# Optimization experiments

Hardware: AMD Instinct MI355X
Metric: run time of the kernel (lower is better)

Reference implementation:

```python
import jax, jax.numpy as jnp
import numpy as np

N = 120000   # hits
K = 512      # non-noise objects (ids 1..K; id 0 = noise)
D = 8        # cluster-space dim
C = 6        # pid classes
Q_MIN = 1.0
NOISE_THR = 0
PAYLOAD_W = 1.0
EPS = 1e-9


def setup_inputs() -> dict:
    key = jax.random.key(0)
    ks = jax.random.split(key, 9)
    beta = jax.random.uniform(ks[0], (N,), dtype=jnp.float32) * 0.95 + 0.01  # keep arctanh finite
    x = jax.random.normal(ks[1], (N, D), dtype=jnp.float32)
    object_id = jax.random.randint(ks[2], (N,), 0, K + 1).astype(jnp.int32)
    # guarantee every object id (and noise id 0) appears at least once
    object_id = object_id.at[: K + 1].set(jnp.arange(K + 1, dtype=jnp.int32))
    energy = jax.random.normal(ks[3], (N,), dtype=jnp.float32)
    energy_per_hit = jax.random.normal(ks[4], (N,), dtype=jnp.float32)
    momentum = jax.random.normal(ks[5], (N, 3), dtype=jnp.float32)
    momentum_per_hit = jax.random.normal(ks[6], (N, 3), dtype=jnp.float32)
    pid_logits = jax.random.normal(ks[7], (N, C), dtype=jnp.float32)
    pid_per_hit = jax.random.randint(ks[8], (N,), 0, C).astype(jnp.int32)
    return dict(beta=beta, x=x, object_id=object_id, energy=energy,
                energy_per_hit=energy_per_hit, momentum=momentum,
                momentum_per_hit=momentum_per_hit, pid_logits=pid_logits,
                pid_per_hit=pid_per_hit)


def _oc_core(beta, x, object_id):
    """condensation_loss_tiger with weights=1, max_n_rep=0 (no repulsive sampling)."""
    oids = jnp.arange(1, K + 1, dtype=object_id.dtype)
    att_mask = object_id[:, None] == oids[None, :]              # [N, K]
    q = jnp.arctanh(beta) ** 2 + Q_MIN                          # [N]
    alphas = jnp.argmax(q[:, None] * att_mask, axis=0)          # [K] condensation points
    x_k = x[alphas]                                             # [K, D]
    q_k = q[alphas]                                             # [K]
    # squared euclidean distance via gemm (avoids [N,K,D] intermediate)
    d2 = (jnp.sum(x * x, axis=1)[:, None] + jnp.sum(x_k * x_k, axis=1)[None, :]
          - 2.0 * (x @ x_k.T))
    d2 = jnp.maximum(d2, 0.0)                                   # [N, K]
    dist = jnp.sqrt(jnp.maximum(d2, 1e-12))
    qw = q[:, None] * q_k[None, :]                              # [N, K]
    # attractive: per-object normalized by hits in object, then mean over objects
    att_norm = jnp.sum(att_mask, axis=0).astype(x.dtype)        # [K]
    v_att = jnp.sum(jnp.where(att_mask, qw * d2, 0.0) / (att_norm + EPS)[None, :]) / K
    # repulsive: hinge (1 - dist), normalized by n_hits not in object
    rep_mask = (~att_mask) & (dist < 1.0)
    n_rep_k = jnp.sum(~att_mask, axis=0).astype(x.dtype)        # [K]
    n_rep = jnp.sum(rep_mask)
    v_rep = jnp.sum(jnp.where(rep_mask, qw * (1.0 - dist), 0.0) / (n_rep_k + EPS)[None, :]) / K
    l_coward = jnp.mean(1.0 - beta[alphas])
    noise_m = (object_id <= NOISE_THR).astype(beta.dtype)
    l_noise = jnp.sum(beta * noise_m) / jnp.sum(noise_m)
    return v_att, v_rep, l_coward, l_noise, n_rep


def reference(beta, x, object_id, energy, energy_per_hit, momentum,
              momentum_per_hit, pid_logits, pid_per_hit):
    v_att, v_rep, l_coward, l_noise, n_rep = _oc_core(beta, x, object_id)
    oc_total = v_att + v_rep + l_coward + l_noise
    # payload losses on non-noise hits (masked means == F.*_loss on gathered rows)
    m = (object_id > NOISE_THR).astype(beta.dtype)              # [N]
    nm = jnp.sum(m)
    e_loss = jnp.sum((energy - energy_per_hit) ** 2 * m) / nm
    p_loss = jnp.sum((momentum - momentum_per_hit) ** 2 * m[:, None]) / (nm * momentum.shape[1])
    logp = jax.nn.log_softmax(pid_logits, axis=-1)              # [N, C]
    nll = -jnp.take_along_axis(logp, pid_per_hit[:, None], axis=1)[:, 0]
    pid_loss = jnp.sum(nll * m) / nm
    total = oc_total + PAYLOAD_W * (e_loss + p_loss + pid_loss)
    return (v_att, v_rep, l_coward, l_noise, n_rep.astype(jnp.float32),
            oc_total, e_loss, p_loss, pid_loss, total)
```

## Files before the change

### kernel.cpp

```cpp
#include <hip/hip_runtime.h>
#include <math.h>

#define KOBJ 512
#define KTW 8
#define TK 32
#define NTILE (KOBJ / TK)
#define HB 8
#define HCH (256 * HB)
#define MPREP 256
#define GB 64

typedef _Float16 half2_t __attribute__((ext_vector_type(2)));

#define AGS(p, v) __hip_atomic_store((p), (v), __ATOMIC_RELAXED, __HIP_MEMORY_SCOPE_AGENT)
#define AGL(p)    __hip_atomic_load((p), __ATOMIC_RELAXED, __HIP_MEMORY_SCOPE_AGENT)

__device__ __forceinline__ float wave_red_f(float v) {
  #pragma unroll
  for (int off = 32; off > 0; off >>= 1) v += __shfl_down(v, off, 64);
  return v;
}

__device__ __forceinline__ float q_of_beta(float b) {
  float a = 0.5f * __logf((1.f + b) / (1.f - b));
  return fmaf(a, a, 1.f);
}

__device__ __forceinline__ float dot8h(uint4 kx, const uint* y, float acc) {
#if __has_builtin(__builtin_amdgcn_fdot2)
  acc = __builtin_amdgcn_fdot2(__builtin_bit_cast(half2_t, y[0]),
                               __builtin_bit_cast(half2_t, kx.x), acc, false);
  acc = __builtin_amdgcn_fdot2(__builtin_bit_cast(half2_t, y[1]),
                               __builtin_bit_cast(half2_t, kx.y), acc, false);
  acc = __builtin_amdgcn_fdot2(__builtin_bit_cast(half2_t, y[2]),
                               __builtin_bit_cast(half2_t, kx.z), acc, false);
  acc = __builtin_amdgcn_fdot2(__builtin_bit_cast(half2_t, y[3]),
                               __builtin_bit_cast(half2_t, kx.w), acc, false);
#else
  const uint kk[4] = {kx.x, kx.y, kx.z, kx.w};
  #pragma unroll
  for (int c = 0; c < 4; c++) {
    half2_t a = __builtin_bit_cast(half2_t, y[c]);
    half2_t b = __builtin_bit_cast(half2_t, kk[c]);
    acc = fmaf((float)a.x, (float)b.x, acc);
    acc = fmaf((float)a.y, (float)b.y, acc);
  }
#endif
  return acc;
}

__global__ __launch_bounds__(256) void
k_prep(const float* __restrict__ beta, const float* __restrict__ x,
       const int* __restrict__ oid,
       const float* __restrict__ energy, const float* __restrict__ eph,
       const float* __restrict__ mom, const float* __restrict__ mph,
       const float* __restrict__ logits, const int* __restrict__ pid,
       unsigned long long* __restrict__ amax_part,
       unsigned* __restrict__ cnt_part,
       float* __restrict__ scal_part,
       uint4* __restrict__ hry, uint4* __restrict__ hrm,
       unsigned* __restrict__ done_cnt, int n) {
  __shared__ unsigned long long lmax[KOBJ];
  __shared__ unsigned lcnt[KOBJ];
  if (blockIdx.x == 0 && threadIdx.x == 0) *done_cnt = 0u;
  for (int t = threadIdx.x; t < KOBJ; t += 256) { lmax[t] = 0ull; lcnt[t] = 0u; }
  __syncthreads();

  const float4* xp = (const float4*)x;
  float e_t = 0.f, p_t = 0.f, pid_t = 0.f, noise_t = 0.f, ncnt = 0.f, mcnt = 0.f;
  for (int i = blockIdx.x * 256 + threadIdx.x; i < n; i += MPREP * 256) {
    float b = beta[i];
    int o = oid[i];
    float q = q_of_beta(b);
    float4 xa = xp[2 * (size_t)i];
    float4 xb = xp[2 * (size_t)i + 1];
    float xi[8] = {xa.x, xa.y, xa.z, xa.w, xb.x, xb.y, xb.z, xb.w};
    float s = 0.f;
    #pragma unroll
    for (int c = 0; c < 8; c++) s = fmaf(xi[c], xi[c], s);
    uint4 r0;
    {
      half2_t h0 = { (_Float16)(-2.f * xi[0]), (_Float16)(-2.f * xi[1]) };
      half2_t h1 = { (_Float16)(-2.f * xi[2]), (_Float16)(-2.f * xi[3]) };
      half2_t h2 = { (_Float16)(-2.f * xi[4]), (_Float16)(-2.f * xi[5]) };
      half2_t h3 = { (_Float16)(-2.f * xi[6]), (_Float16)(-2.f * xi[7]) };
      r0.x = __builtin_bit_cast(uint, h0);
      r0.y = __builtin_bit_cast(uint, h1);
      r0.z = __builtin_bit_cast(uint, h2);
      r0.w = __builtin_bit_cast(uint, h3);
    }
    uint4 r1 = { __float_as_uint(s), __float_as_uint(q), (uint)o, 0u };
    hry[i] = r0;
    hrm[i] = r1;

    if (o > 0) {
      unsigned long long key = ((unsigned long long)__float_as_uint(q) << 32)
                             | (unsigned long long)(unsigned)(~(unsigned)i);
      atomicMax(&lmax[o - 1], key);
      atomicAdd(&lcnt[o - 1], 1u);
      mcnt += 1.f;
      float de = energy[i] - eph[i];
      e_t = fmaf(de, de, e_t);
      float p0 = mom[3*i+0] - mph[3*i+0];
      float p1 = mom[3*i+1] - mph[3*i+1];
      float p2 = mom[3*i+2] - mph[3*i+2];
      p_t = fmaf(p0, p0, p_t); p_t = fmaf(p1, p1, p_t); p_t = fmaf(p2, p2, p_t);
      const float* lg = logits + 6*i;
      float l0=lg[0], l1=lg[1], l2=lg[2], l3=lg[3], l4=lg[4], l5=lg[5];
      float mx = fmaxf(fmaxf(fmaxf(l0,l1),fmaxf(l2,l3)), fmaxf(l4,l5));
      float sm = __expf(l0-mx)+__expf(l1-mx)+__expf(l2-mx)
               + __expf(l3-mx)+__expf(l4-mx)+__expf(l5-mx);
      int pc = pid[i];
      float lp = (pc==0)?l0:(pc==1)?l1:(pc==2)?l2:(pc==3)?l3:(pc==4)?l4:l5;
      pid_t += mx + __logf(sm) - lp;
    } else {
      noise_t += b;
      ncnt += 1.f;
    }
  }
  __syncthreads();

  for (int t = threadIdx.x; t < KOBJ; t += 256) {
    amax_part[(size_t)blockIdx.x * KOBJ + t] = lmax[t];
    cnt_part[(size_t)blockIdx.x * KOBJ + t]  = lcnt[t];
  }

  float vals[6] = {e_t, p_t, pid_t, noise_t, ncnt, mcnt};
  #pragma unroll
  for (int j = 0; j < 6; j++) vals[j] = wave_red_f(vals[j]);
  __shared__ float sred[4][6];
  int w = threadIdx.x >> 6, l = threadIdx.x & 63;
  if (l == 0) {
    #pragma unroll
    for (int j = 0; j < 6; j++) sred[w][j] = vals[j];
  }
  __syncthreads();
  if (threadIdx.x == 0) {
    #pragma unroll
    for (int j = 0; j < 6; j++)
      scal_part[blockIdx.x * 8 + j] = sred[0][j]+sred[1][j]+sred[2][j]+sred[3][j];
  }
}

__global__ __launch_bounds__(256) void
k_gather(const float* __restrict__ x, const float* __restrict__ beta,
         const unsigned long long* __restrict__ amax_part,
         const unsigned* __restrict__ cnt_part,
         uint* __restrict__ ktab, float* __restrict__ cow_part, int n) {
  __shared__ unsigned long long skey[32][8];
  __shared__ unsigned scnt[32][8];
  const int o = threadIdx.x & 7, seg = threadIdx.x >> 3;
  const int k = blockIdx.x * 8 + o;

  unsigned long long key = 0ull;
  unsigned cnt = 0u;
  for (int m = seg; m < MPREP; m += 32) {
    unsigned long long km = amax_part[(size_t)m * KOBJ + k];
    key = (km > key) ? km : key;
    cnt += cnt_part[(size_t)m * KOBJ + k];
  }
  skey[seg][o] = key;
  scnt[seg][o] = cnt;
  __syncthreads();
  for (int s = 16; s > 0; s >>= 1) {
    if (seg < s) {
      unsigned long long k2 = skey[seg + s][o];
      if (k2 > skey[seg][o]) skey[seg][o] = k2;
      scnt[seg][o] += scnt[seg + s][o];
    }
    __syncthreads();
  }

  float cowv = 0.f;
  if (threadIdx.x < 8) {
    key = skey[0][o];
    cnt = scnt[0][o];
    unsigned idx = ~(unsigned)(key & 0xffffffffull);
    float q_k = __uint_as_float((unsigned)(key >> 32));
    const float4* xp = (const float4*)x;
    float4 xa = xp[2 * (size_t)idx];
    float4 xb = xp[2 * (size_t)idx + 1];
    float xv[8] = {xa.x, xa.y, xa.z, xa.w, xb.x, xb.y, xb.z, xb.w};
    float s2 = 0.f;
    #pragma unroll
    for (int c = 0; c < 8; c++) s2 = fmaf(xv[c], xv[c], s2);
    uint* kt = ktab + (size_t)k * KTW;
    #pragma unroll
    for (int c = 0; c < 4; c++) {
      half2_t hp = { (_Float16)xv[2*c], (_Float16)xv[2*c+1] };
      kt[c] = __builtin_bit_cast(uint, hp);
    }
    kt[4] = __float_as_uint(s2);
    kt[5] = __float_as_uint(q_k / ((float)(n - (int)cnt) + 1e-9f));
    kt[6] = __float_as_uint(q_k / ((float)cnt + 1e-9f));
    kt[7] = 0u;
    cowv = 1.f - beta[idx];
  }
  if (threadIdx.x < 64) {
    cowv = wave_red_f(cowv);
    if (threadIdx.x == 0) cow_part[blockIdx.x] = cowv;
  }
}

__global__ __launch_bounds__(256, 4) void
k_pairs(const uint4* __restrict__ hry, const uint4* __restrict__ hrm,
        const uint* __restrict__ ktab,
        const float* __restrict__ scal_part, const float* __restrict__ cow_part,
        float* __restrict__ pairs_part, unsigned* __restrict__ done_cnt,
        float* __restrict__ out, int n) {
  __shared__ __align__(16) uint skt[(TK + 1) * KTW];
  __shared__ float sredu[4][10];
  __shared__ unsigned slast;
  const int tid = threadIdx.x;
  const int w = tid >> 6, l = tid & 63;
  const int tile0 = blockIdx.y * TK;
  const int hbase = blockIdx.x * HCH;
  const int nblk = gridDim.x * gridDim.y;
  const int bid = blockIdx.y * gridDim.x + blockIdx.x;

  skt[tid] = ktab[(size_t)tile0 * KTW + tid];
  if (tid < KTW) skt[TK * KTW + tid] = 0u;
  __syncthreads();

  uint yh[HB][4];
  float thr[HB], bh[HB], qi[HB];
  int own[HB];
  #pragma unroll
  for (int h = 0; h < HB; h++) {
    int i = hbase + h * 256 + tid;
    if (i < n) {
      uint4 ra = hry[i];
      uint4 rb = hrm[i];
      yh[h][0] = ra.x; yh[h][1] = ra.y; yh[h][2] = ra.z; yh[h][3] = ra.w;
      float s = __uint_as_float(rb.x);
      bh[h] = s;
      thr[h] = 1.f - s;
      qi[h] = __uint_as_float(rb.y);
      own[h] = (int)rb.z - 1 - tile0;
    } else {
      #pragma unroll
      for (int c = 0; c < 4; c++) yh[h][c] = 0u;
      bh[h] = 0.f;
      thr[h] = -1e30f;
      qi[h] = 0.f;
      own[h] = -1;
    }
  }

  float att = 0.f, rep = 0.f, nrep = 0.f;
  const uint4* skt4 = (const uint4*)skt;
  uint4 ka = skt4[0], kb = skt4[1];
  #pragma unroll 2
  for (int r = 0; r < TK; r++) {
    uint4 na = skt4[2*r + 2];
    uint4 nb = skt4[2*r + 3];
    float s2 = __uint_as_float(kb.x);
    float wr = __uint_as_float(kb.y);
    float dp[HB];
    #pragma unroll
    for (int h = 0; h < HB; h++) dp[h] = dot8h(ka, yh[h], s2);
    bool any = false;
    #pragma unroll
    for (int h = 0; h < HB; h++) any = any | (dp[h] < thr[h]);
    if (any) {
      #pragma unroll
      for (int h = 0; h < HB; h++) {
        if (dp[h] < thr[h]) {
          float d2 = dp[h] + bh[h];
          float dist = sqrtf(fmaxf(d2, 1e-12f));
          rep = fmaf(qi[h] * (1.f - dist), wr, rep);
          nrep += 1.f;
        }
      }
    }
    ka = na; kb = nb;
  }

  #pragma unroll
  for (int h = 0; h < HB; h++) {
    int ko = own[h];
    if (ko >= 0 && ko < TK) {
      uint4 oa = skt4[2*ko];
      uint4 ob = skt4[2*ko + 1];
      float s2 = __uint_as_float(ob.x);
      float wr = __uint_as_float(ob.y);
      float wa = __uint_as_float(ob.z);
      float dp = dot8h(oa, yh[h], s2);
      float d2 = dp + bh[h];
      att = fmaf(qi[h] * fmaxf(d2, 0.f), wa, att);
      if (dp < thr[h]) {
        float dist = sqrtf(fmaxf(d2, 1e-12f));
        rep = fmaf(-qi[h] * (1.f - dist), wr, rep);
        nrep -= 1.f;
      }
    }
  }

  att = wave_red_f(att);
  rep = wave_red_f(rep);
  nrep = wave_red_f(nrep);
  if (l == 0) { sredu[w][0] = att; sredu[w][1] = rep; sredu[w][2] = nrep; }
  __syncthreads();
  if (tid == 0) {
    AGS(&pairs_part[bid * 4 + 0], sredu[0][0]+sredu[1][0]+sredu[2][0]+sredu[3][0]);
    AGS(&pairs_part[bid * 4 + 1], sredu[0][1]+sredu[1][1]+sredu[2][1]+sredu[3][1]);
    AGS(&pairs_part[bid * 4 + 2], sredu[0][2]+sredu[1][2]+sredu[2][2]+sredu[3][2]);
    slast = __hip_atomic_fetch_add(done_cnt, 1u, __ATOMIC_ACQ_REL,
                                   __HIP_MEMORY_SCOPE_AGENT);
  }
  __syncthreads();

  if (slast == (unsigned)(nblk - 1)) {
    float v[10] = {0,0,0,0,0,0,0,0,0,0};
    for (int b2 = tid; b2 < nblk; b2 += 256) {
      v[0] += AGL(&pairs_part[b2 * 4 + 0]);
      v[1] += AGL(&pairs_part[b2 * 4 + 1]);
      v[2] += AGL(&pairs_part[b2 * 4 + 2]);
    }
    for (int m = tid; m < MPREP; m += 256) {
      #pragma unroll
      for (int j = 0; j < 6; j++) v[3 + j] += scal_part[m * 8 + j];
    }
    for (int g = tid; g < GB; g += 256) v[9] += cow_part[g];
    #pragma unroll
    for (int j = 0; j < 10; j++) v[j] = wave_red_f(v[j]);
    __syncthreads();
    if (l == 0) {
      #pragma unroll
      for (int j = 0; j < 10; j++) sredu[w][j] = v[j];
    }
    __syncthreads();
    if (tid == 0) {
      float t10[10];
      #pragma unroll
      for (int j = 0; j < 10; j++)
        t10[j] = sredu[0][j]+sredu[1][j]+sredu[2][j]+sredu[3][j];
      float v_att  = t10[0] / (float)KOBJ;
      float v_rep  = t10[1] / (float)KOBJ;
      float n_rep  = t10[2];
      float l_cow  = t10[9] / (float)KOBJ;
      float l_noise = t10[6] / t10[7];
      float oc = v_att + v_rep + l_cow + l_noise;
      float nm = t10[8];
      float e_loss  = t10[3] / nm;
      float p_loss  = t10[4] / (nm * 3.f);
      float pid_loss = t10[5] / nm;
      out[0] = v_att;
      out[1] = v_rep;
      out[2] = l_cow;
      out[3] = l_noise;
      out[4] = n_rep;
      out[5] = oc;
      out[6] = e_loss;
      out[7] = p_loss;
      out[8] = pid_loss;
      out[9] = oc + e_loss + p_loss + pid_loss;
    }
  }
}

extern "C" void kernel_launch(void* const* d_in, const int* in_sizes, int n_in,
                              void* d_out, int out_size, void* d_ws, size_t ws_size,
                              hipStream_t stream) {
  const float* beta   = (const float*)d_in[0];
  const float* x      = (const float*)d_in[1];
  const int*   oid    = (const int*)d_in[2];
  const float* energy = (const float*)d_in[3];
  const float* eph    = (const float*)d_in[4];
  const float* mom    = (const float*)d_in[5];
  const float* mph    = (const float*)d_in[6];
  const float* logits = (const float*)d_in[7];
  const int*   pid    = (const int*)d_in[8];
  float* outp = (float*)d_out;
  const int n = in_sizes[0];
  const int nhb = (n + HCH - 1) / HCH;
  const int nblk_tot = nhb * NTILE;

  char* base = (char*)d_ws;
  size_t off = 0;
  uint*  ktab       = (uint*)(base + off);  off += (size_t)KOBJ * KTW * 4;
  float* cow_part   = (float*)(base + off); off += (size_t)GB * 4;
  float* pairs_part = (float*)(base + off); off += (size_t)nblk_tot * 4 * 4;
  float* scal_part  = (float*)(base + off); off += (size_t)MPREP * 8 * 4;
  unsigned* done_cnt = (unsigned*)(base + off); off += 256;
  off = (off + 255) & ~(size_t)255;
  unsigned long long* amax_part = (unsigned long long*)(base + off); off += (size_t)MPREP * KOBJ * 8;
  unsigned* cnt_part = (unsigned*)(base + off);                      off += (size_t)MPREP * KOBJ * 4;
  off = (off + 255) & ~(size_t)255;
  uint4* hry = (uint4*)(base + off); off += (size_t)nhb * HCH * 16;
  uint4* hrm = (uint4*)(base + off); off += (size_t)nhb * HCH * 16;

  k_prep<<<MPREP, 256, 0, stream>>>(beta, x, oid, energy, eph, mom, mph, logits, pid,
                                    amax_part, cnt_part, scal_part, hry, hrm,
                                    done_cnt, n);
  k_gather<<<GB, 256, 0, stream>>>(x, beta, amax_part, cnt_part, ktab, cow_part, n);
  k_pairs<<<dim3(nhb, NTILE), 256, 0, stream>>>(hry, hrm, ktab, scal_part, cow_part,
                                                pairs_part, done_cnt, outp, n);
}
```

Measured before the change: 112.8 us.

## Drop gather kernel; use replicated global atomic tables and rebuild object table per block

The prep kernel now handles one hit per thread and updates condensation-point argmax keys and per-object counts with global atomics into 8 replicated tables, chosen by block index. This replaces the 256 per-block partial tables that k_gather then reduced. k_gather is removed: each k_pairs block merges the 8 tables for its 32-object tile, gathers the condensation points and builds its shared object table itself, and the coward term is reduced per tile. A memset zeroes the tables and the done counter, which saves one kernel launch and the large partial-table traffic. In exchange it adds global atomic contention and redundant per-block gather work.

Measured after the change: 119.7 us. +6.1%, slower.

```diff
diff --git a/kernel.cpp b/kernel.cpp
--- a/kernel.cpp
+++ b/kernel.cpp
@@ -7,8 +7,7 @@
 #define NTILE (KOBJ / TK)
 #define HB 8
 #define HCH (256 * HB)
-#define MPREP 256
-#define GB 64
+#define NTAB 8
 
 typedef _Float16 half2_t __attribute__((ext_vector_type(2)));
 
@@ -55,23 +54,20 @@
        const float* __restrict__ energy, const float* __restrict__ eph,
        const float* __restrict__ mom, const float* __restrict__ mph,
        const float* __restrict__ logits, const int* __restrict__ pid,
-       unsigned long long* __restrict__ amax_part,
-       unsigned* __restrict__ cnt_part,
+       unsigned long long* __restrict__ amax8,
+       unsigned* __restrict__ cnt8,
        float* __restrict__ scal_part,
-       uint4* __restrict__ hry, uint4* __restrict__ hrm,
-       unsigned* __restrict__ done_cnt, int n) {
-  __shared__ unsigned long long lmax[KOBJ];
-  __shared__ unsigned lcnt[KOBJ];
-  if (blockIdx.x == 0 && threadIdx.x == 0) *done_cnt = 0u;
-  for (int t = threadIdx.x; t < KOBJ; t += 256) { lmax[t] = 0ull; lcnt[t] = 0u; }
-  __syncthreads();
-
-  const float4* xp = (const float4*)x;
+       uint4* __restrict__ hry, uint4* __restrict__ hrm, int n) {
+  const int tid = threadIdx.x;
+  const int i = blockIdx.x * 256 + tid;
+  const int tb = blockIdx.x & (NTAB - 1);
+
   float e_t = 0.f, p_t = 0.f, pid_t = 0.f, noise_t = 0.f, ncnt = 0.f, mcnt = 0.f;
-  for (int i = blockIdx.x * 256 + threadIdx.x; i < n; i += MPREP * 256) {
+  if (i < n) {
     float b = beta[i];
     int o = oid[i];
     float q = q_of_beta(b);
+    const float4* xp = (const float4*)x;
     float4 xa = xp[2 * (size_t)i];
     float4 xb = xp[2 * (size_t)i + 1];
     float xi[8] = {xa.x, xa.y, xa.z, xa.w, xb.x, xb.y, xb.z, xb.w};
@@ -96,119 +92,58 @@
     if (o > 0) {
       unsigned long long key = ((unsigned long long)__float_as_uint(q) << 32)
                              | (unsigned long long)(unsigned)(~(unsigned)i);
-      atomicMax(&lmax[o - 1], key);
-      atomicAdd(&lcnt[o - 1], 1u);
-      mcnt += 1.f;
+      atomicMax(&amax8[(size_t)tb * KOBJ + (o - 1)], key);
+      atomicAdd(&cnt8[(size_t)tb * KOBJ + (o - 1)], 1u);
+      mcnt = 1.f;
       float de = energy[i] - eph[i];
-      e_t = fmaf(de, de, e_t);
+      e_t = de * de;
       float p0 = mom[3*i+0] - mph[3*i+0];
       float p1 = mom[3*i+1] - mph[3*i+1];
       float p2 = mom[3*i+2] - mph[3*i+2];
-      p_t = fmaf(p0, p0, p_t); p_t = fmaf(p1, p1, p_t); p_t = fmaf(p2, p2, p_t);
-      const float* lg = logits + 6*i;
-      float l0=lg[0], l1=lg[1], l2=lg[2], l3=lg[3], l4=lg[4], l5=lg[5];
+      p_t = fmaf(p0, p0, 0.f); p_t = fmaf(p1, p1, p_t); p_t = fmaf(p2, p2, p_t);
+      const float2* lg2 = (const float2*)(logits + 6*i);
+      float2 la = lg2[0], lb = lg2[1], lc = lg2[2];
+      float l0=la.x, l1=la.y, l2=lb.x, l3=lb.y, l4=lc.x, l5=lc.y;
       float mx = fmaxf(fmaxf(fmaxf(l0,l1),fmaxf(l2,l3)), fmaxf(l4,l5));
       float sm = __expf(l0-mx)+__expf(l1-mx)+__expf(l2-mx)
                + __expf(l3-mx)+__expf(l4-mx)+__expf(l5-mx);
       int pc = pid[i];
       float lp = (pc==0)?l0:(pc==1)?l1:(pc==2)?l2:(pc==3)?l3:(pc==4)?l4:l5;
-      pid_t += mx + __logf(sm) - lp;
+      pid_t = mx + __logf(sm) - lp;
     } else {
-      noise_t += b;
-      ncnt += 1.f;
-    }
-  }
-  __syncthreads();
-
-  for (int t = threadIdx.x; t < KOBJ; t += 256) {
-    amax_part[(size_t)blockIdx.x * KOBJ + t] = lmax[t];
-    cnt_part[(size_t)blockIdx.x * KOBJ + t]  = lcnt[t];
+      noise_t = b;
+      ncnt = 1.f;
+    }
   }
 
   float vals[6] = {e_t, p_t, pid_t, noise_t, ncnt, mcnt};
   #pragma unroll
   for (int j = 0; j < 6; j++) vals[j] = wave_red_f(vals[j]);
   __shared__ float sred[4][6];
-  int w = threadIdx.x >> 6, l = threadIdx.x & 63;
+  int w = tid >> 6, l = tid & 63;
   if (l == 0) {
     #pragma unroll
     for (int j = 0; j < 6; j++) sred[w][j] = vals[j];
   }
   __syncthreads();
-  if (threadIdx.x == 0) {
+  if (tid == 0) {
     #pragma unroll
     for (int j = 0; j < 6; j++)
       scal_part[blockIdx.x * 8 + j] = sred[0][j]+sred[1][j]+sred[2][j]+sred[3][j];
   }
 }
 
-__global__ __launch_bounds__(256) void
-k_gather(const float* __restrict__ x, const float* __restrict__ beta,
-         const unsigned long long* __restrict__ amax_part,
-         const unsigned* __restrict__ cnt_part,
-         uint* __restrict__ ktab, float* __restrict__ cow_part, int n) {
-  __shared__ unsigned long long skey[32][8];
-  __shared__ unsigned scnt[32][8];
-  const int o = threadIdx.x & 7, seg = threadIdx.x >> 3;
-  const int k = blockIdx.x * 8 + o;
-
-  unsigned long long key = 0ull;
-  unsigned cnt = 0u;
-  for (int m = seg; m < MPREP; m += 32) {
-    unsigned long long km = amax_part[(size_t)m * KOBJ + k];
-    key = (km > key) ? km : key;
-    cnt += cnt_part[(size_t)m * KOBJ + k];
-  }
-  skey[seg][o] = key;
-  scnt[seg][o] = cnt;
-  __syncthreads();
-  for (int s = 16; s > 0; s >>= 1) {
-    if (seg < s) {
-      unsigned long long k2 = skey[seg + s][o];
-      if (k2 > skey[seg][o]) skey[seg][o] = k2;
-      scnt[seg][o] += scnt[seg + s][o];
-    }
-    __syncthreads();
-  }
-
-  float cowv = 0.f;
-  if (threadIdx.x < 8) {
-    key = skey[0][o];
-    cnt = scnt[0][o];
-    unsigned idx = ~(unsigned)(key & 0xffffffffull);
-    float q_k = __uint_as_float((unsigned)(key >> 32));
-    const float4* xp = (const float4*)x;
-    float4 xa = xp[2 * (size_t)idx];
-    float4 xb = xp[2 * (size_t)idx + 1];
-    float xv[8] = {xa.x, xa.y, xa.z, xa.w, xb.x, xb.y, xb.z, xb.w};
-    float s2 = 0.f;
-    #pragma unroll
-    for (int c = 0; c < 8; c++) s2 = fmaf(xv[c], xv[c], s2);
-    uint* kt = ktab + (size_t)k * KTW;
-    #pragma unroll
-    for (int c = 0; c < 4; c++) {
-      half2_t hp = { (_Float16)xv[2*c], (_Float16)xv[2*c+1] };
-      kt[c] = __builtin_bit_cast(uint, hp);
-    }
-    kt[4] = __float_as_uint(s2);
-    kt[5] = __float_as_uint(q_k / ((float)(n - (int)cnt) + 1e-9f));
-    kt[6] = __float_as_uint(q_k / ((float)cnt + 1e-9f));
-    kt[7] = 0u;
-    cowv = 1.f - beta[idx];
-  }
-  if (threadIdx.x < 64) {
-    cowv = wave_red_f(cowv);
-    if (threadIdx.x == 0) cow_part[blockIdx.x] = cowv;
-  }
-}
-
 __global__ __launch_bounds__(256, 4) void
 k_pairs(const uint4* __restrict__ hry, const uint4* __restrict__ hrm,
-        const uint* __restrict__ ktab,
-        const float* __restrict__ scal_part, const float* __restrict__ cow_part,
+        const unsigned long long* __restrict__ amax8,
+        const unsigned* __restrict__ cnt8,
+        const float* __restrict__ x, const float* __restrict__ beta,
+        const float* __restrict__ scal_part, float* __restrict__ cow_part,
         float* __restrict__ pairs_part, unsigned* __restrict__ done_cnt,
-        float* __restrict__ out, int n) {
+        float* __restrict__ out, int n, int nprep) {
   __shared__ __align__(16) uint skt[(TK + 1) * KTW];
+  __shared__ unsigned long long skey[NTAB][TK];
+  __shared__ unsigned scnt[NTAB][TK];
   __shared__ float sredu[4][10];
   __shared__ unsigned slast;
   const int tid = threadIdx.x;
@@ -218,9 +153,49 @@
   const int nblk = gridDim.x * gridDim.y;
   const int bid = blockIdx.y * gridDim.x + blockIdx.x;
 
-  skt[tid] = ktab[(size_t)tile0 * KTW + tid];
-  if (tid < KTW) skt[TK * KTW + tid] = 0u;
-  __syncthreads();
+  {
+    const int tb = tid >> 5, ko = tid & 31;
+    skey[tb][ko] = amax8[(size_t)tb * KOBJ + tile0 + ko];
+    scnt[tb][ko] = cnt8[(size_t)tb * KOBJ + tile0 + ko];
+    __syncthreads();
+    float cowv = 0.f;
+    if (tid < TK) {
+      unsigned long long key = skey[0][tid];
+      unsigned cnt = scnt[0][tid];
+      #pragma unroll
+      for (int c = 1; c < NTAB; c++) {
+        unsigned long long kc = skey[c][tid];
+        key = (kc > key) ? kc : key;
+        cnt += scnt[c][tid];
+      }
+      unsigned idx = ~(unsigned)(key & 0xffffffffull);
+      float q_k = __uint_as_float((unsigned)(key >> 32));
+      const float4* xp4 = (const float4*)x;
+      float4 xa = xp4[2 * (size_t)idx];
+      float4 xb = xp4[2 * (size_t)idx + 1];
+      float xv[8] = {xa.x, xa.y, xa.z, xa.w, xb.x, xb.y, xb.z, xb.w};
+      float s2 = 0.f;
+      #pragma unroll
+      for (int c = 0; c < 8; c++) s2 = fmaf(xv[c], xv[c], s2);
+      uint* kt = &skt[tid * KTW];
+      #pragma unroll
+      for (int c = 0; c < 4; c++) {
+        half2_t hp = { (_Float16)xv[2*c], (_Float16)xv[2*c+1] };
+        kt[c] = __builtin_bit_cast(uint, hp);
+      }
+      kt[4] = __float_as_uint(s2);
+      kt[5] = __float_as_uint(q_k / ((float)(n - (int)cnt) + 1e-9f));
+      kt[6] = __float_as_uint(q_k / ((float)cnt + 1e-9f));
+      kt[7] = 0u;
+      if (blockIdx.x == 0) cowv = 1.f - beta[idx];
+    }
+    if (tid >= TK && tid < TK + KTW) skt[TK * KTW + (tid - TK)] = 0u;
+    if (tid < 64) {
+      cowv = wave_red_f(cowv);
+      if (tid == 0 && blockIdx.x == 0) AGS(&cow_part[blockIdx.y], cowv);
+    }
+    __syncthreads();
+  }
 
   uint yh[HB][4];
   float thr[HB], bh[HB], qi[HB];
@@ -317,11 +292,11 @@
       v[1] += AGL(&pairs_part[b2 * 4 + 1]);
       v[2] += AGL(&pairs_part[b2 * 4 + 2]);
     }
-    for (int m = tid; m < MPREP; m += 256) {
+    for (int m = tid; m < nprep; m += 256) {
       #pragma unroll
       for (int j = 0; j < 6; j++) v[3 + j] += scal_part[m * 8 + j];
     }
-    for (int g = tid; g < GB; g += 256) v[9] += cow_part[g];
+    for (int g = tid; g < NTILE; g += 256) v[9] += AGL(&cow_part[g]);
     #pragma unroll
     for (int j = 0; j < 10; j++) v[j] = wave_red_f(v[j]);
     __syncthreads();
@@ -373,27 +348,28 @@
   const int*   pid    = (const int*)d_in[8];
   float* outp = (float*)d_out;
   const int n = in_sizes[0];
+  const int nprep = (n + 255) / 256;
   const int nhb = (n + HCH - 1) / HCH;
   const int nblk_tot = nhb * NTILE;
 
   char* base = (char*)d_ws;
   size_t off = 0;
-  uint*  ktab       = (uint*)(base + off);  off += (size_t)KOBJ * KTW * 4;
-  float* cow_part   = (float*)(base + off); off += (size_t)GB * 4;
+  unsigned long long* amax8 = (unsigned long long*)(base + off); off += (size_t)NTAB * KOBJ * 8;
+  unsigned* cnt8     = (unsigned*)(base + off);                  off += (size_t)NTAB * KOBJ * 4;
+  unsigned* done_cnt = (unsigned*)(base + off);                  off += 4;
+  const size_t zero_bytes = off;
+  off = (off + 255) & ~(size_t)255;
+  float* cow_part   = (float*)(base + off); off += (size_t)NTILE * 4;
   float* pairs_part = (float*)(base + off); off += (size_t)nblk_tot * 4 * 4;
-  float* scal_part  = (float*)(base + off); off += (size_t)MPREP * 8 * 4;
-  unsigned* done_cnt = (unsigned*)(base + off); off += 256;
+  float* scal_part  = (float*)(base + off); off += (size_t)nprep * 8 * 4;
   off = (off + 255) & ~(size_t)255;
-  unsigned long long* amax_part = (unsigned long long*)(base + off); off += (size_t)MPREP * KOBJ * 8;
-  unsigned* cnt_part = (unsigned*)(base + off);                      off += (size_t)MPREP * KOBJ * 4;
-  off = (off + 255) & ~(size_t)255;
-  uint4* hry = (uint4*)(base + off); off += (size_t)nhb * HCH * 16;
-  uint4* hrm = (uint4*)(base + off); off += (size_t)nhb * HCH * 16;
-
-  k_prep<<<MPREP, 256, 0, stream>>>(beta, x, oid, energy, eph, mom, mph, logits, pid,
-                                    amax_part, cnt_part, scal_part, hry, hrm,
-                                    done_cnt, n);
-  k_gather<<<GB, 256, 0, stream>>>(x, beta, amax_part, cnt_part, ktab, cow_part, n);
-  k_pairs<<<dim3(nhb, NTILE), 256, 0, stream>>>(hry, hrm, ktab, scal_part, cow_part,
-                                                pairs_part, done_cnt, outp, n);
-}
+  uint4* hry = (uint4*)(base + off); off += (size_t)nprep * 256 * 16;
+  uint4* hrm = (uint4*)(base + off); off += (size_t)nprep * 256 * 16;
+
+  hipMemsetAsync(base, 0, zero_bytes, stream);
+  k_prep<<<nprep, 256, 0, stream>>>(beta, x, oid, energy, eph, mom, mph, logits, pid,
+                                    amax8, cnt8, scal_part, hry, hrm, n);
+  k_pairs<<<dim3(nhb, NTILE), 256, 0, stream>>>(hry, hrm, amax8, cnt8, x, beta,
+                                                scal_part, cow_part, pairs_part,
+                                                done_cnt, outp, n, nprep);
+}
```

## Compute pairwise distance margins with MFMA 32x32x16 f16 instead of fdot2 loops

Applied to the files above, without the earlier changes.

Replaces the per-thread packed-half dot-product loop over the 32 objects in a tile with an MFMA 32x32x16 f16 instruction. Each hit row and object column is augmented so that the matrix product directly yields d2-1, which serves as the repulsion test. Hit data is staged in LDS so lanes can build MFMA fragments, the same-object exclusion moves into the hinge path via a reload of hrm, and launch bounds drop to 3 blocks per SU. The aim is to cut VALU dot-product work, at the cost of more LDS, lower occupancy, f16 rounding of s-1 and s2 in the threshold test, and scattered global reloads when pairs pass the threshold.

Measured after the change: 119.5 us. +5.9%, slower.

```diff
diff --git a/kernel.cpp b/kernel.cpp
--- a/kernel.cpp
+++ b/kernel.cpp
@@ -5,12 +5,13 @@
 #define KTW 8
 #define TK 32
 #define NTILE (KOBJ / TK)
-#define HB 8
-#define HCH (256 * HB)
+#define HCH 2048
 #define MPREP 256
 #define GB 64
 
 typedef _Float16 half2_t __attribute__((ext_vector_type(2)));
+typedef _Float16 f16x8   __attribute__((ext_vector_type(8)));
+typedef float    f32x16  __attribute__((ext_vector_type(16)));
 
 #define AGS(p, v) __hip_atomic_store((p), (v), __ATOMIC_RELAXED, __HIP_MEMORY_SCOPE_AGENT)
 #define AGL(p)    __hip_atomic_load((p), __ATOMIC_RELAXED, __HIP_MEMORY_SCOPE_AGENT)
@@ -89,7 +90,9 @@
       r0.z = __builtin_bit_cast(uint, h2);
       r0.w = __builtin_bit_cast(uint, h3);
     }
-    uint4 r1 = { __float_as_uint(s), __float_as_uint(q), (uint)o, 0u };
+    half2_t hb1 = { (_Float16)(s - 1.f), (_Float16)1.f };
+    uint4 r1 = { __float_as_uint(s), __float_as_uint(q), (uint)o,
+                 __builtin_bit_cast(uint, hb1) };
     hry[i] = r0;
     hrm[i] = r1;
 
@@ -193,7 +196,8 @@
     kt[4] = __float_as_uint(s2);
     kt[5] = __float_as_uint(q_k / ((float)(n - (int)cnt) + 1e-9f));
     kt[6] = __float_as_uint(q_k / ((float)cnt + 1e-9f));
-    kt[7] = 0u;
+    half2_t h1s = { (_Float16)1.f, (_Float16)s2 };
+    kt[7] = __builtin_bit_cast(uint, h1s);
     cowv = 1.f - beta[idx];
   }
   if (threadIdx.x < 64) {
@@ -202,15 +206,18 @@
   }
 }
 
-__global__ __launch_bounds__(256, 4) void
+__global__ __launch_bounds__(256, 3) void
 k_pairs(const uint4* __restrict__ hry, const uint4* __restrict__ hrm,
         const uint* __restrict__ ktab,
         const float* __restrict__ scal_part, const float* __restrict__ cow_part,
         float* __restrict__ pairs_part, unsigned* __restrict__ done_cnt,
         float* __restrict__ out, int n) {
-  __shared__ __align__(16) uint skt[(TK + 1) * KTW];
+  __shared__ __align__(16) uint4 yls[HCH];
+  __shared__ uint bh1s[HCH];
+  __shared__ __align__(16) uint skt[TK * KTW];
   __shared__ float sredu[4][10];
   __shared__ unsigned slast;
+
   const int tid = threadIdx.x;
   const int w = tid >> 6, l = tid & 63;
   const int tile0 = blockIdx.y * TK;
@@ -219,80 +226,84 @@
   const int bid = blockIdx.y * gridDim.x + blockIdx.x;
 
   skt[tid] = ktab[(size_t)tile0 * KTW + tid];
-  if (tid < KTW) skt[TK * KTW + tid] = 0u;
-  __syncthreads();
-
-  uint yh[HB][4];
-  float thr[HB], bh[HB], qi[HB];
-  int own[HB];
+
+  uint4 yl[8];
+  float bhv[8], qv[8];
+  int ov[8];
   #pragma unroll
-  for (int h = 0; h < HB; h++) {
-    int i = hbase + h * 256 + tid;
+  for (int j = 0; j < 8; j++) {
+    int il = j * 256 + tid;
+    int i = hbase + il;
+    uint4 ry, rm;
     if (i < n) {
-      uint4 ra = hry[i];
-      uint4 rb = hrm[i];
-      yh[h][0] = ra.x; yh[h][1] = ra.y; yh[h][2] = ra.z; yh[h][3] = ra.w;
-      float s = __uint_as_float(rb.x);
-      bh[h] = s;
-      thr[h] = 1.f - s;
-      qi[h] = __uint_as_float(rb.y);
-      own[h] = (int)rb.z - 1 - tile0;
+      ry = hry[i];
+      rm = hrm[i];
     } else {
+      ry = (uint4){0u, 0u, 0u, 0u};
+      half2_t sent = { (_Float16)60000.f, (_Float16)0.f };
+      rm = (uint4){0u, 0u, 0u, __builtin_bit_cast(uint, sent)};
+    }
+    yls[il] = ry;
+    bh1s[il] = rm.w;
+    yl[j] = ry;
+    bhv[j] = __uint_as_float(rm.x);
+    qv[j] = __uint_as_float(rm.y);
+    ov[j] = (int)rm.z - 1;
+  }
+  __syncthreads();
+
+  const int col = l & 31;
+  uint4 bfr;
+  if (l < 32) bfr = *(const uint4*)&skt[col * KTW];
+  else        bfr = (uint4){skt[col * KTW + 7], 0u, 0u, 0u};
+  const float wr = __uint_as_float(skt[col * KTW + 5]);
+  const int cglob = tile0 + col;
+  const f16x8 Bf = __builtin_bit_cast(f16x8, bfr);
+  const f32x16 zc = {0.f,0.f,0.f,0.f,0.f,0.f,0.f,0.f,
+                     0.f,0.f,0.f,0.f,0.f,0.f,0.f,0.f};
+
+  float att = 0.f, rep = 0.f, nrep = 0.f;
+  for (int hb = w * 16; hb < w * 16 + 16; hb++) {
+    const int rbase = hb * 32;
+    uint4 afr;
+    if (l < 32) afr = yls[rbase + col];
+    else        afr = (uint4){bh1s[rbase + col], 0u, 0u, 0u};
+    f32x16 acc = __builtin_amdgcn_mfma_f32_32x32x16_f16(
+        __builtin_bit_cast(f16x8, afr), Bf, zc, 0, 0, 0);
+
+    float m = acc[0];
+    #pragma unroll
+    for (int r2 = 1; r2 < 16; r2++) m = fminf(m, acc[r2]);
+    if (__any(m < 0.f)) {
       #pragma unroll
-      for (int c = 0; c < 4; c++) yh[h][c] = 0u;
-      bh[h] = 0.f;
-      thr[h] = -1e30f;
-      qi[h] = 0.f;
-      own[h] = -1;
-    }
-  }
-
-  float att = 0.f, rep = 0.f, nrep = 0.f;
-  const uint4* skt4 = (const uint4*)skt;
-  uint4 ka = skt4[0], kb = skt4[1];
-  #pragma unroll 2
-  for (int r = 0; r < TK; r++) {
-    uint4 na = skt4[2*r + 2];
-    uint4 nb = skt4[2*r + 3];
-    float s2 = __uint_as_float(kb.x);
-    float wr = __uint_as_float(kb.y);
-    float dp[HB];
-    #pragma unroll
-    for (int h = 0; h < HB; h++) dp[h] = dot8h(ka, yh[h], s2);
-    bool any = false;
-    #pragma unroll
-    for (int h = 0; h < HB; h++) any = any | (dp[h] < thr[h]);
-    if (any) {
-      #pragma unroll
-      for (int h = 0; h < HB; h++) {
-        if (dp[h] < thr[h]) {
-          float d2 = dp[h] + bh[h];
+      for (int reg = 0; reg < 16; reg++) {
+        float t = acc[reg];
+        if (t < 0.f) {
+          int row = (reg & 3) + 8 * (reg >> 2) + 4 * (l >> 5);
+          uint4 hv = hrm[hbase + rbase + row];
+          float d2 = t + 1.f;
           float dist = sqrtf(fmaxf(d2, 1e-12f));
-          rep = fmaf(qi[h] * (1.f - dist), wr, rep);
-          nrep += 1.f;
+          if ((int)hv.z - 1 != cglob) {
+            rep = fmaf(__uint_as_float(hv.y) * (1.f - dist), wr, rep);
+            nrep += 1.f;
+          }
         }
       }
     }
-    ka = na; kb = nb;
   }
 
   #pragma unroll
-  for (int h = 0; h < HB; h++) {
-    int ko = own[h];
+  for (int h = 0; h < 8; h++) {
+    int ko = ov[h] - tile0;
     if (ko >= 0 && ko < TK) {
-      uint4 oa = skt4[2*ko];
-      uint4 ob = skt4[2*ko + 1];
-      float s2 = __uint_as_float(ob.x);
-      float wr = __uint_as_float(ob.y);
-      float wa = __uint_as_float(ob.z);
-      float dp = dot8h(oa, yh[h], s2);
-      float d2 = dp + bh[h];
-      att = fmaf(qi[h] * fmaxf(d2, 0.f), wa, att);
-      if (dp < thr[h]) {
-        float dist = sqrtf(fmaxf(d2, 1e-12f));
-        rep = fmaf(-qi[h] * (1.f - dist), wr, rep);
-        nrep -= 1.f;
-      }
+      const uint* kr = &skt[ko * KTW];
+      uint4 kx = *(const uint4*)kr;
+      float s2 = __uint_as_float(kr[4]);
+      float wa = __uint_as_float(kr[6]);
+      uint yy[4] = {yl[h].x, yl[h].y, yl[h].z, yl[h].w};
+      float dp = dot8h(kx, yy, s2);
+      float d2 = dp + bhv[h];
+      att = fmaf(qv[h] * fmaxf(d2, 0.f), wa, att);
     }
   }
 
@@ -317,9 +328,9 @@
       v[1] += AGL(&pairs_part[b2 * 4 + 1]);
       v[2] += AGL(&pairs_part[b2 * 4 + 2]);
     }
-    for (int m = tid; m < MPREP; m += 256) {
+    for (int m2 = tid; m2 < MPREP; m2 += 256) {
       #pragma unroll
-      for (int j = 0; j < 6; j++) v[3 + j] += scal_part[m * 8 + j];
+      for (int j = 0; j < 6; j++) v[3 + j] += scal_part[m2 * 8 + j];
     }
     for (int g = tid; g < GB; g += 256) v[9] += cow_part[g];
     #pragma unroll
```
